# Optimization experiments

Hardware: AMD Instinct MI355X
Metric: run time of the kernel (lower is better)

The kernel has to match this reference:

```python
import jax, jax.numpy as jnp
import numpy as np

E = 768       # embed dim
NH = 12       # heads
HD = 64       # head dim
WIN = 14      # window size
DEPTH = 12
PATCH = 16
WINDOW_IDX = (0, 1, 3, 4, 6, 7, 9, 10)
EPS = 1e-6


def layer_norm(x, w, b):
    mu = jnp.mean(x, axis=-1, keepdims=True)
    var = jnp.mean(jnp.square(x - mu), axis=-1, keepdims=True)
    return (x - mu) * jax.lax.rsqrt(var + EPS) * w + b


def get_rel_pos(size, rel_pos):
    # q_size == k_size -> direct lookup, no interpolation
    coords = jnp.arange(size)
    rel = coords[:, None] - coords[None, :] + (size - 1)
    return rel_pos[rel]  # (size, size, HD)


def attention(x, qkv_w, qkv_b, proj_w, proj_b, rel_h, rel_w):
    B, H, W, _ = x.shape
    N = H * W
    qkv = (x.reshape(B, N, E) @ qkv_w + qkv_b).reshape(B, N, 3, NH, HD)
    q = qkv[:, :, 0].transpose(0, 2, 1, 3).reshape(B * NH, N, HD)
    k = qkv[:, :, 1].transpose(0, 2, 1, 3).reshape(B * NH, N, HD)
    v = qkv[:, :, 2].transpose(0, 2, 1, 3).reshape(B * NH, N, HD)
    attn = (q * (HD ** -0.5)) @ k.transpose(0, 2, 1)  # (B*NH, N, N)
    # decomposed relative position bias
    Rh = get_rel_pos(H, rel_h)  # (H, H, HD)
    Rw = get_rel_pos(W, rel_w)  # (W, W, HD)
    r_q = q.reshape(B * NH, H, W, HD)
    rh = jnp.einsum('bhwc,hkc->bhwk', r_q, Rh)
    rw = jnp.einsum('bhwc,wkc->bhwk', r_q, Rw)
    attn = attn.reshape(B * NH, H, W, H, W) + rh[:, :, :, :, None] + rw[:, :, :, None, :]
    attn = jax.nn.softmax(attn.reshape(B * NH, N, N), axis=-1)
    out = (attn @ v).reshape(B, NH, H, W, HD).transpose(0, 2, 3, 1, 4).reshape(B, H, W, E)
    return out @ proj_w + proj_b


def window_partition(x, ws):
    B, H, W, C = x.shape
    pad_h, pad_w = (-H) % ws, (-W) % ws
    x = jnp.pad(x, ((0, 0), (0, pad_h), (0, pad_w), (0, 0)))
    Hp, Wp = H + pad_h, W + pad_w
    x = x.reshape(B, Hp // ws, ws, Wp // ws, ws, C).transpose(0, 1, 3, 2, 4, 5)
    return x.reshape(-1, ws, ws, C), (Hp, Wp)


def window_unpartition(win, ws, pad_hw, hw):
    Hp, Wp = pad_hw
    H, W = hw
    B = win.shape[0] // ((Hp // ws) * (Wp // ws))
    x = win.reshape(B, Hp // ws, Wp // ws, ws, ws, -1).transpose(0, 1, 3, 2, 4, 5)
    return x.reshape(B, Hp, Wp, -1)[:, :H, :W]


def _forward(x, patch_w, patch_b, pos_embed,
             ln1_w, ln1_b, qkv_w, qkv_b, proj_w, proj_b,
             rel_h_win, rel_w_win, rel_h_glob, rel_w_glob,
             ln2_w, ln2_b, fc1_w, fc1_b, fc2_w, fc2_b, out_w, out_b):
    # patch embed: conv 16x16 stride 16
    x = jax.lax.conv_general_dilated(
        x, patch_w, (PATCH, PATCH), 'VALID',
        dimension_numbers=('NCHW', 'OIHW', 'NCHW'))
    x = x.transpose(0, 2, 3, 1) + patch_b  # (B, H, W, C)
    x = x + pos_embed
    win_i, glob_i = 0, 0
    for i in range(DEPTH):
        shortcut = x
        h = layer_norm(x, ln1_w[i], ln1_b[i])
        if i in WINDOW_IDX:
            hw = h.shape[1:3]
            h, pad_hw = window_partition(h, WIN)
            h = attention(h, qkv_w[i], qkv_b[i], proj_w[i], proj_b[i],
                          rel_h_win[win_i], rel_w_win[win_i])
            h = window_unpartition(h, WIN, pad_hw, hw)
            win_i += 1
        else:
            h = attention(h, qkv_w[i], qkv_b[i], proj_w[i], proj_b[i],
                          rel_h_glob[glob_i], rel_w_glob[glob_i])
            glob_i += 1
        x = shortcut + h
        h = layer_norm(x, ln2_w[i], ln2_b[i])
        h = jax.nn.gelu(h @ fc1_w[i] + fc1_b[i], approximate=False) @ fc2_w[i] + fc2_b[i]
        x = x + h
    feat = x.transpose(0, 3, 1, 2)  # (B, C, H, W) == 'last_feat'
    return jnp.einsum('bchw,oc->bohw', feat, out_w) + out_b[None, :, None, None]


def setup_inputs() -> dict:
    key = jax.random.key(0)
    ks = iter(jax.random.split(key, 64))
    def n(shape, s=0.02):
        return jax.random.normal(next(ks), shape, jnp.float32) * s
    B, IMG = 2, 512
    G = IMG // PATCH  # 32
    return {
        'x': jax.random.normal(next(ks), (B, 3, IMG, IMG), jnp.float32),
        'patch_w': n((E, 3, PATCH, PATCH)),
        'patch_b': jnp.zeros((E,), jnp.float32),
        'pos_embed': n((1, G, G, E)),
        'ln1_w': jnp.ones((DEPTH, E), jnp.float32),
        'ln1_b': jnp.zeros((DEPTH, E), jnp.float32),
        'qkv_w': n((DEPTH, E, 3 * E)),
        'qkv_b': jnp.zeros((DEPTH, 3 * E), jnp.float32),
        'proj_w': n((DEPTH, E, E)),
        'proj_b': jnp.zeros((DEPTH, E), jnp.float32),
        'rel_h_win': n((8, 2 * WIN - 1, HD)),
        'rel_w_win': n((8, 2 * WIN - 1, HD)),
        'rel_h_glob': n((4, 2 * G - 1, HD)),
        'rel_w_glob': n((4, 2 * G - 1, HD)),
        'ln2_w': jnp.ones((DEPTH, E), jnp.float32),
        'ln2_b': jnp.zeros((DEPTH, E), jnp.float32),
        'fc1_w': n((DEPTH, E, 4 * E)),
        'fc1_b': jnp.zeros((DEPTH, 4 * E), jnp.float32),
        'fc2_w': n((DEPTH, 4 * E, E)),
        'fc2_b': jnp.zeros((DEPTH, E), jnp.float32),
        'out_w': n((256, E)),
        'out_b': jnp.zeros((256,), jnp.float32),
    }


def reference(x, patch_w, patch_b, pos_embed,
              ln1_w, ln1_b, qkv_w, qkv_b, proj_w, proj_b,
              rel_h_win, rel_w_win, rel_h_glob, rel_w_glob,
              ln2_w, ln2_b, fc1_w, fc1_b, fc2_w, fc2_b, out_w, out_b):
    return _forward(x, patch_w, patch_b, pos_embed,
                    ln1_w, ln1_b, qkv_w, qkv_b, proj_w, proj_b,
                    rel_h_win, rel_w_win, rel_h_glob, rel_w_glob,
                    ln2_w, ln2_b, fc1_w, fc1_b, fc2_w, fc2_b, out_w, out_b)
```

## Files before the change

kernel.cpp:

```cpp
#include <hip/hip_runtime.h>
#include <hip/hip_bf16.h>
#include <math.h>

static constexpr int E   = 768;
static constexpr int NH  = 12;
static constexpr int HD  = 64;
static constexpr int Bsz = 2;
static constexpr int G   = 32;
static constexpr int NTOK = G * G;
static constexpr int ROWS = Bsz * NTOK;
static constexpr int WS  = 14;
static constexpr int NWIN_SIDE = 3;
static constexpr int NWIN = NWIN_SIDE * NWIN_SIDE;
static constexpr int BW  = Bsz * NWIN;
static constexpr int NW  = WS * WS;
static constexpr int WROWS = BW * NW;
static constexpr int WIN_MASK = 0x6DB;

typedef __attribute__((ext_vector_type(8))) short short8;
typedef __attribute__((ext_vector_type(4))) float f32x4;
typedef unsigned short ushort_t;

__device__ __forceinline__ unsigned short f2bf(float x) {
  union { float f; unsigned u; } v; v.f = x;
  unsigned r = v.u + 0x7fffu + ((v.u >> 16) & 1u);
  return (unsigned short)(r >> 16);
}
__device__ __forceinline__ float bf2f(unsigned short h) {
  union { unsigned u; float f; } v; v.u = ((unsigned)h) << 16;
  return v.f;
}

__device__ __forceinline__ void glds16(const void* g, void* l) {
  __builtin_amdgcn_global_load_lds(
      (const __attribute__((address_space(1))) unsigned*)g,
      (__attribute__((address_space(3))) unsigned*)l, 16, 0, 0);
}

__global__ __launch_bounds__(256) void ln_kernel(
    const float* __restrict__ in, const float* __restrict__ w,
    const float* __restrict__ b, ushort_t* __restrict__ out) {
  const int wave = threadIdx.x >> 6, lane = threadIdx.x & 63;
  const int row = blockIdx.x * 4 + wave;
  const float4* r4 = (const float4*)(in + (size_t)row * E);
  float4 v[3];
  v[0] = r4[lane]; v[1] = r4[lane + 64]; v[2] = r4[lane + 128];
  float s = 0.f, s2 = 0.f;
#pragma unroll
  for (int i = 0; i < 3; i++) {
    s += v[i].x + v[i].y + v[i].z + v[i].w;
    s2 += v[i].x * v[i].x + v[i].y * v[i].y + v[i].z * v[i].z + v[i].w * v[i].w;
  }
#pragma unroll
  for (int off = 1; off <= 32; off <<= 1) {
    s += __shfl_xor(s, off);
    s2 += __shfl_xor(s2, off);
  }
  const float mean = s * (1.f / E);
  const float var  = s2 * (1.f / E) - mean * mean;
  const float rs   = rsqrtf(var + 1e-6f);
  ushort_t* o = out + (size_t)row * E;
#pragma unroll
  for (int i = 0; i < 3; i++) {
    const int e0 = (lane + i * 64) * 4;
    ushort4 p;
    p.x = f2bf((v[i].x - mean) * rs * w[e0]     + b[e0]);
    p.y = f2bf((v[i].y - mean) * rs * w[e0 + 1] + b[e0 + 1]);
    p.z = f2bf((v[i].z - mean) * rs * w[e0 + 2] + b[e0 + 2]);
    p.w = f2bf((v[i].w - mean) * rs * w[e0 + 3] + b[e0 + 3]);
    *(ushort4*)&o[e0] = p;
  }
}

enum { OP_QKV = 0, OP_GELU = 1, OP_ADD = 2, OP_POS = 3, OP_HEAD = 4 };

template <int OP>
__global__ __launch_bounds__(256) void gemm_128(
    const ushort_t* __restrict__ A, const ushort_t* __restrict__ Bt,
    const float* __restrict__ bias, const float* __restrict__ res,
    const float* __restrict__ pos, void* __restrict__ Cp,
    int M, int N, int K, int ncol) {
  __shared__ ushort_t As[128 * 64];
  __shared__ ushort_t Bs[128 * 64];
  const int tid = threadIdx.x, wave = tid >> 6, lane = tid & 63;
  const int lx = lane & 15, ly = lane >> 4;

  const int nwg = gridDim.x;
  const int q = nwg >> 3, r = nwg & 7;
  const int xcd = blockIdx.x & 7, loc = blockIdx.x >> 3;
  const int wgid = ((xcd < r) ? xcd * (q + 1) : r * (q + 1) + (xcd - r) * q) + loc;
  const int brow = wgid / ncol, bcol = wgid - brow * ncol;
  const int row0 = brow * 128, col0 = bcol * 128;
  const int wm = (wave >> 1) * 64, wn = (wave & 1) * 64;
  const int rin = lane >> 3, pseg = lane & 7;
  const int lseg = pseg ^ rin;
  f32x4 acc[4][4] = {};

  const ushort_t* aptr[4];
  const ushort_t* bptr[4];
#pragma unroll
  for (int j = 0; j < 4; j++) {
    const int instr = wave * 4 + j;
    int ar = row0 + instr * 8 + rin;
    if (ar >= M) ar = M - 1;
    aptr[j] = &A[(size_t)ar * K + lseg * 8];
    const int br = col0 + instr * 8 + rin;
    bptr[j] = &Bt[(size_t)br * K + lseg * 8];
  }

  for (int k0 = 0; k0 < K; k0 += 64) {
    __syncthreads();
#pragma unroll
    for (int j = 0; j < 4; j++) {
      const int instr = wave * 4 + j;
      glds16(aptr[j] + k0, &As[instr * 512]);
      glds16(bptr[j] + k0, &Bs[instr * 512]);
    }
    __syncthreads();
#pragma unroll
    for (int kb = 0; kb < 2; kb++) {
      short8 af[4], bfm[4];
#pragma unroll
      for (int m = 0; m < 4; m++) {
        const int rr = wm + m * 16 + lx;
        af[m] = *(const short8*)&As[rr * 64 + (((kb * 4 + ly) ^ (rr & 7)) * 8)];
      }
#pragma unroll
      for (int n = 0; n < 4; n++) {
        const int rr = wn + n * 16 + lx;
        bfm[n] = *(const short8*)&Bs[rr * 64 + (((kb * 4 + ly) ^ (rr & 7)) * 8)];
      }
      __builtin_amdgcn_s_setprio(1);
#pragma unroll
      for (int m = 0; m < 4; m++)
#pragma unroll
        for (int n = 0; n < 4; n++)
          acc[m][n] = __builtin_amdgcn_mfma_f32_16x16x32_bf16(af[m], bfm[n], acc[m][n], 0, 0, 0);
      __builtin_amdgcn_s_setprio(0);
    }
  }

#pragma unroll
  for (int m = 0; m < 4; m++) {
#pragma unroll
    for (int r4 = 0; r4 < 4; r4++) {
      const int gr = row0 + wm + m * 16 + ly * 4 + r4;
      if (gr >= M) continue;
#pragma unroll
      for (int n = 0; n < 4; n++) {
        const int gc = col0 + wn + n * 16 + lx;
        float v = acc[m][n][r4] + bias[gc];
        if (OP == OP_GELU) v = 0.5f * v * (1.f + erff(v * 0.70710678118654752f));
        if (OP == OP_ADD)  v += res[(size_t)gr * N + gc];
        if (OP == OP_QKV || OP == OP_GELU)
          ((ushort_t*)Cp)[(size_t)gr * N + gc] = f2bf(v);
        else
          ((float*)Cp)[(size_t)gr * N + gc] = v;
      }
    }
  }
}

template <int OP, int MAP>
__global__ __launch_bounds__(256) void gemm_bt(
    const ushort_t* __restrict__ A, const ushort_t* __restrict__ Bt,
    const float* __restrict__ bias, const float* __restrict__ res,
    const float* __restrict__ pos, void* __restrict__ Cp,
    int M, int N, int K, int ncol) {
  __shared__ ushort_t As[2][64 * 64];
  __shared__ ushort_t Bs[2][64 * 64];
  const int tid = threadIdx.x, wave = tid >> 6, lane = tid & 63;
  const int lx = lane & 15, ly = lane >> 4;

  const int nwg = gridDim.x;
  const int q = nwg >> 3, r = nwg & 7;
  const int xcd = blockIdx.x & 7, loc = blockIdx.x >> 3;
  const int wgid = ((xcd < r) ? xcd * (q + 1) : r * (q + 1) + (xcd - r) * q) + loc;
  const int brow = wgid / ncol, bcol = wgid - brow * ncol;
  const int row0 = brow * 64, col0 = bcol * 64;
  const int wm = (wave >> 1) * 32, wn = (wave & 1) * 32;
  const int rin = lane >> 3, pseg = lane & 7;
  const int lseg = pseg ^ rin;
  f32x4 acc[2][2] = {};

  const ushort_t* aptr[2];
  const ushort_t* bptr[2];
#pragma unroll
  for (int j = 0; j < 2; j++) {
    const int slot = wave * 2 + j;
    int ar = row0 + slot * 8 + rin;
    if (ar >= M) ar = M - 1;
    if (MAP == 2) {
      const int bI = ar >> 10, t = ar & 1023, y = t >> 5, x = t & 31;
      const int by = y / WS, wy = y - by * WS;
      const int bx = x / WS, wx = x - bx * WS;
      const int win = bI * NWIN + by * NWIN_SIDE + bx;
      aptr[j] = &A[((size_t)win * NW + wy * WS + wx) * E + lseg * 8];
    } else {
      aptr[j] = &A[(size_t)ar * K + lseg * 8];
    }
    const int br = col0 + slot * 8 + rin;
    bptr[j] = &Bt[(size_t)br * K + lseg * 8];
  }

#pragma unroll
  for (int j = 0; j < 2; j++) {
    const int slot = wave * 2 + j;
    glds16(aptr[j], &As[0][slot * 512]);
    glds16(bptr[j], &Bs[0][slot * 512]);
  }

  const int nt = K >> 6;
  for (int t = 0; t < nt; t++) {
    const int cur = t & 1;
    if (t + 1 < nt) {
      const int k1 = (t + 1) << 6;
#pragma unroll
      for (int j = 0; j < 2; j++) {
        const int slot = wave * 2 + j;
        glds16(aptr[j] + k1, &As[cur ^ 1][slot * 512]);
        glds16(bptr[j] + k1, &Bs[cur ^ 1][slot * 512]);
      }
      asm volatile("s_waitcnt vmcnt(4)" ::: "memory");
    } else {
      asm volatile("s_waitcnt vmcnt(0)" ::: "memory");
    }
    __builtin_amdgcn_s_barrier();
    __builtin_amdgcn_sched_barrier(0);
#pragma unroll
    for (int kb = 0; kb < 2; kb++) {
      short8 af[2], bfm[2];
#pragma unroll
      for (int m = 0; m < 2; m++) {
        const int rr = wm + m * 16 + lx;
        af[m] = *(const short8*)&As[cur][rr * 64 + (((kb * 4 + ly) ^ (rr & 7)) * 8)];
      }
#pragma unroll
      for (int n = 0; n < 2; n++) {
        const int rr = wn + n * 16 + lx;
        bfm[n] = *(const short8*)&Bs[cur][rr * 64 + (((kb * 4 + ly) ^ (rr & 7)) * 8)];
      }
      __builtin_amdgcn_s_setprio(1);
#pragma unroll
      for (int m = 0; m < 2; m++)
#pragma unroll
        for (int n = 0; n < 2; n++)
          acc[m][n] = __builtin_amdgcn_mfma_f32_16x16x32_bf16(af[m], bfm[n], acc[m][n], 0, 0, 0);
      __builtin_amdgcn_s_setprio(0);
    }
    asm volatile("s_waitcnt lgkmcnt(0)" ::: "memory");
    __builtin_amdgcn_s_barrier();
    __builtin_amdgcn_sched_barrier(0);
  }

#pragma unroll
  for (int m = 0; m < 2; m++) {
#pragma unroll
    for (int r4 = 0; r4 < 4; r4++) {
      const int gr = row0 + wm + m * 16 + ly * 4 + r4;
      if (gr >= M) continue;
#pragma unroll
      for (int n = 0; n < 2; n++) {
        const int gc = col0 + wn + n * 16 + lx;
        float v = acc[m][n][r4] + bias[gc];
        if (OP == OP_GELU) v = 0.5f * v * (1.f + erff(v * 0.70710678118654752f));
        if (OP == OP_ADD)  v += res[(size_t)gr * N + gc];
        if (OP == OP_POS)  v += pos[(size_t)(gr & 1023) * N + gc];
        if (OP == OP_QKV || OP == OP_GELU)
          ((ushort_t*)Cp)[(size_t)gr * N + gc] = f2bf(v);
        else if (OP == OP_HEAD)
          ((float*)Cp)[(((size_t)(gr >> 10) * 256 + gc) << 10) | (gr & 1023)] = v;
        else
          ((float*)Cp)[(size_t)gr * N + gc] = v;
      }
    }
  }
}

__global__ __launch_bounds__(128) void attn_mfma(
    const ushort_t* __restrict__ qkv, ushort_t* __restrict__ out,
    const float* __restrict__ relh, const float* __restrict__ relw,
    int Hd, int Wd) {
  const int Ntok = Hd * Wd;
  __shared__ ushort_t smem[11392];
  ushort_t* Ks   = smem;
  ushort_t* Vst  = smem + 2048;
  ushort_t* Ps   = smem + 4608;
  ushort_t* Qs   = smem;
  ushort_t* RelS = smem + 2048;
  ushort_t* Th   = smem + 6144;
  ushort_t* Tw   = smem + 8256;
  ushort_t* khw  = smem + 10368;

  const int tid = threadIdx.x, wave = tid >> 6, lane = tid & 63;
  const int lx = lane & 15, ly = lane >> 4;
  const int bh = blockIdx.y, b = bh / NH, nh = bh % NH;
  const int q0 = blockIdx.x * 32;
  const size_t base = (size_t)b * Ntok * 2304 + nh * 64;

#pragma unroll
  for (int i = 0; i < 2; i++) {
    const int fv = i * 128 + tid;
    const int row = fv >> 3, dv8 = (fv & 7) * 8;
    const int qq = min(q0 + row, Ntok - 1);
    short8 v = *(const short8*)&qkv[base + (size_t)qq * 2304 + dv8];
    *(short8*)&Qs[(row * 64 + dv8) ^ ((row & 7) << 3)] = v;
  }
  for (int k = tid; k < 1024; k += 128) {
    const int kc = min(k, Ntok - 1);
    const int kh = kc / Wd;
    khw[k] = (ushort_t)((kh << 8) | (kc - kh * Wd));
  }
  __syncthreads();

  short8 qa[2];
  {
    const int row = wave * 16 + lx;
#pragma unroll
    for (int kb = 0; kb < 2; kb++)
      qa[kb] = *(const short8*)&Qs[(row * 64 + kb * 32 + ly * 8) ^ ((row & 7) << 3)];
  }
  int qh_r[4], qw_r[4];
#pragma unroll
  for (int r = 0; r < 4; r++) {
    const int qc = min(q0 + wave * 16 + ly * 4 + r, Ntok - 1);
    qh_r[r] = qc / Wd;
    qw_r[r] = qc - qh_r[r] * Wd;
  }

  for (int t = 0; t < 2; t++) {
    const float* rel = t ? relw : relh;
    const int TR = t ? (2 * Wd - 1) : (2 * Hd - 1);
    __syncthreads();
#pragma unroll
    for (int i = 0; i < 4; i++) {
      const int fv = i * 128 + tid;
      const int row = fv >> 3, c8 = (fv & 7) * 8;
      short8 v = {};
      if (row < TR) {
        const float* rp = &rel[(size_t)row * 64 + c8];
        const float4 a = *(const float4*)rp;
        const float4 bq = *(const float4*)(rp + 4);
        v[0] = (short)f2bf(a.x);  v[1] = (short)f2bf(a.y);
        v[2] = (short)f2bf(a.z);  v[3] = (short)f2bf(a.w);
        v[4] = (short)f2bf(bq.x); v[5] = (short)f2bf(bq.y);
        v[6] = (short)f2bf(bq.z); v[7] = (short)f2bf(bq.w);
      }
      *(short8*)&RelS[(row * 64 + c8) ^ ((row & 7) << 3)] = v;
    }
    __syncthreads();
    const int NT = (TR + 15) >> 4;
    ushort_t* T = t ? Tw : Th;
    for (int nt = 0; nt < NT; nt++) {
      f32x4 a = {};
      __builtin_amdgcn_s_setprio(1);
#pragma unroll
      for (int kb = 0; kb < 2; kb++) {
        const int rrow = nt * 16 + lx;
        short8 bfv = *(const short8*)&RelS[(rrow * 64 + kb * 32 + ly * 8) ^ ((rrow & 7) << 3)];
        a = __builtin_amdgcn_mfma_f32_16x16x32_bf16(qa[kb], bfv, a, 0, 0, 0);
      }
      __builtin_amdgcn_s_setprio(0);
#pragma unroll
      for (int reg = 0; reg < 4; reg++)
        T[(wave * 16 + ly * 4 + reg) * 66 + nt * 16 + lx] = f2bf(a[reg]);
    }
  }

  f32x4 o[4] = {};
  float m_[4], l_[4];
#pragma unroll
  for (int r = 0; r < 4; r++) { m_[r] = -3e38f; l_[r] = 0.f; }

  const int nkt = (Ntok + 31) >> 5;
  const int srow = tid >> 3, c7 = tid & 7, dv8s = c7 * 8;
  const int vswz = (c7 & 3) << 3;

  short8 kpre[2], vpre[2];
#pragma unroll
  for (int i = 0; i < 2; i++) {
    const int gk = srow + i * 16;
    short8 kv = {}, vv = {};
    if (gk < Ntok) {
      kv = *(const short8*)&qkv[base + 768 + (size_t)gk * 2304 + dv8s];
      vv = *(const short8*)&qkv[base + 1536 + (size_t)gk * 2304 + dv8s];
    }
    kpre[i] = kv; vpre[i] = vv;
  }

  for (int kt = 0; kt < nkt; kt++) {
    __syncthreads();
#pragma unroll
    for (int i = 0; i < 2; i++) {
      const int row = srow + i * 16;
      *(short8*)&Ks[(row * 64 + dv8s) ^ ((row & 7) << 3)] = kpre[i];
      const int kcol = row ^ vswz;
#pragma unroll
      for (int j = 0; j < 8; j++)
        Vst[(dv8s + j) * 40 + kcol] = (ushort_t)vpre[i][j];
    }
    if (kt + 1 < nkt) {
#pragma unroll
      for (int i = 0; i < 2; i++) {
        const int gk = (kt + 1) * 32 + srow + i * 16;
        short8 kv = {}, vv = {};
        if (gk < Ntok) {
          kv = *(const short8*)&qkv[base + 768 + (size_t)gk * 2304 + dv8s];
          vv = *(const short8*)&qkv[base + 1536 + (size_t)gk * 2304 + dv8s];
        }
        kpre[i] = kv; vpre[i] = vv;
      }
    }
    __syncthreads();

    f32x4 c[2] = {};
    __builtin_amdgcn_s_setprio(1);
#pragma unroll
    for (int kb = 0; kb < 2; kb++)
#pragma unroll
      for (int ct = 0; ct < 2; ct++) {
        const int krow = ct * 16 + lx;
        short8 kf = *(const short8*)&Ks[(krow * 64 + kb * 32 + ly * 8) ^ ((krow & 7) << 3)];
        c[ct] = __builtin_amdgcn_mfma_f32_16x16x32_bf16(qa[kb], kf, c[ct], 0, 0, 0);
      }
    __builtin_amdgcn_s_setprio(0);

    const int k0a = kt * 32 + lx, k1a = k0a + 16;
    const int tv0 = khw[k0a], tv1 = khw[k1a];
    const int kh0 = tv0 >> 8, kw0 = tv0 & 255;
    const int kh1 = tv1 >> 8, kw1 = tv1 & 255;
    float pv0[4], pv1[4], mt[4];
#pragma unroll
    for (int r = 0; r < 4; r++) {
      const int trow = (wave * 16 + ly * 4 + r) * 66;
      float s0 = c[0][r] * 0.125f + bf2f(Th[trow + qh_r[r] - kh0 + Hd - 1])
               + bf2f(Tw[trow + qw_r[r] - kw0 + Wd - 1]);
      float s1 = c[1][r] * 0.125f + bf2f(Th[trow + qh_r[r] - kh1 + Hd - 1])
               + bf2f(Tw[trow + qw_r[r] - kw1 + Wd - 1]);
      if (k0a >= Ntok) s0 = -1e30f;
      if (k1a >= Ntok) s1 = -1e30f;
      pv0[r] = s0; pv1[r] = s1;
      mt[r] = fmaxf(s0, s1);
    }
    const float dmax = fmaxf(fmaxf(mt[0] - m_[0], mt[1] - m_[1]),
                             fmaxf(mt[2] - m_[2], mt[3] - m_[3]));
    if (!__all(dmax <= 8.f)) {
#pragma unroll
      for (int r = 0; r < 4; r++) {
        float mr = mt[r];
#pragma unroll
        for (int off = 1; off <= 8; off <<= 1) mr = fmaxf(mr, __shfl_xor(mr, off));
        const float mn = fmaxf(m_[r], mr);
        const float sc = __expf(m_[r] - mn);
        m_[r] = mn; l_[r] *= sc;
#pragma unroll
        for (int dt = 0; dt < 4; dt++) o[dt][r] *= sc;
      }
    }
#pragma unroll
    for (int r = 0; r < 4; r++) {
      const float p0 = __expf(pv0[r] - m_[r]);
      const float p1 = __expf(pv1[r] - m_[r]);
      l_[r] += p0 + p1;
      const int pb = wave * 640 + (ly * 4 + r) * 40;
      Ps[pb + lx]      = f2bf(p0);
      Ps[pb + 16 + lx] = f2bf(p1);
    }
    short8 pf = *(const short8*)&Ps[wave * 640 + lx * 40 + ly * 8];
    __builtin_amdgcn_s_setprio(1);
#pragma unroll
    for (int dt = 0; dt < 4; dt++) {
      const int drow = dt * 16 + lx;
      short8 vf = *(const short8*)&Vst[drow * 40 + ((ly * 8) ^ (((drow >> 3) & 3) << 3))];
      o[dt] = __builtin_amdgcn_mfma_f32_16x16x32_bf16(pf, vf, o[dt], 0, 0, 0);
    }
    __builtin_amdgcn_s_setprio(0);
  }

#pragma unroll
  for (int r = 0; r < 4; r++) {
#pragma unroll
    for (int off = 1; off <= 8; off <<= 1) l_[r] += __shfl_xor(l_[r], off);
    const int qq = q0 + wave * 16 + ly * 4 + r;
    if (qq >= Ntok) continue;
    const float inv = 1.f / l_[r];
#pragma unroll
    for (int dt = 0; dt < 4; dt++)
      out[((size_t)b * Ntok + qq) * E + nh * 64 + dt * 16 + lx] = f2bf(o[dt][r] * inv);
  }
}

__global__ __launch_bounds__(128) void qkv_winpart(
    const ushort_t* __restrict__ qi, const float* __restrict__ qkvb,
    ushort_t* __restrict__ qw) {
  const int row = blockIdx.x;
  const int win = row / NW, t = row - win * NW;
  const int wy = t / WS, wx = t - wy * WS;
  const int b = win / NWIN, wr = win - b * NWIN;
  const int by = wr / NWIN_SIDE, bx = wr - by * NWIN_SIDE;
  const int y = by * WS + wy, x = bx * WS + wx;
  short8* dst = (short8*)(qw + (size_t)row * 2304);
  if (y < G && x < G) {
    const short8* src = (const short8*)(qi + (((size_t)b * G + y) * G + x) * 2304);
    for (int e = threadIdx.x; e < 288; e += 128) dst[e] = src[e];
  } else {
    for (int e = threadIdx.x; e < 288; e += 128) {
      short8 v;
#pragma unroll
      for (int j = 0; j < 8; j++) v[j] = (short)f2bf(qkvb[e * 8 + j]);
      dst[e] = v;
    }
  }
}

__global__ __launch_bounds__(256) void im2col(const float* __restrict__ x,
                                              ushort_t* __restrict__ out) {
  const int blk = blockIdx.x;
  const int b = blk >> 10, t = blk & 1023, gy = t >> 5, gx = t & 31;
  for (int k = threadIdx.x; k < 768; k += 256) {
    const int ci = k >> 8, rem = k & 255, py = rem >> 4, px = rem & 15;
    out[(size_t)blk * 768 + k] =
        f2bf(x[(((size_t)b * 3 + ci) * 512 + gy * 16 + py) * 512 + gx * 16 + px]);
  }
}

__global__ __launch_bounds__(256) void prep_wt64(
    const float* __restrict__ qkvw, const float* __restrict__ projw,
    const float* __restrict__ fc1w, const float* __restrict__ fc2w,
    ushort_t* __restrict__ wq, ushort_t* __restrict__ wp,
    ushort_t* __restrict__ w1, ushort_t* __restrict__ w2) {
  __shared__ float tile[64][65];
  const int blk = blockIdx.x;
  const float* W; ushort_t* Wt; int Kd, Nd, tn, tk;
  if (blk < 432)       { W = qkvw;  Wt = wq; Kd = 768;  Nd = 2304; tn = blk % 36;          tk = blk / 36; }
  else if (blk < 576)  { W = projw; Wt = wp; Kd = 768;  Nd = 768;  tn = (blk - 432) % 12;  tk = (blk - 432) / 12; }
  else if (blk < 1152) { W = fc1w;  Wt = w1; Kd = 768;  Nd = 3072; tn = (blk - 576) % 48;  tk = (blk - 576) / 48; }
  else                 { W = fc2w;  Wt = w2; Kd = 3072; Nd = 768;  tn = (blk - 1152) % 12; tk = (blk - 1152) / 12; }
  const int k0 = tk * 64, n0 = tn * 64;
  const int kr = threadIdx.x >> 2, cg = (threadIdx.x & 3) * 16;
  const float* src = &W[(size_t)(k0 + kr) * Nd + n0 + cg];
#pragma unroll
  for (int j = 0; j < 4; j++) {
    const float4 v = *(const float4*)&src[j * 4];
    tile[kr][cg + j * 4 + 0] = v.x;
    tile[kr][cg + j * 4 + 1] = v.y;
    tile[kr][cg + j * 4 + 2] = v.z;
    tile[kr][cg + j * 4 + 3] = v.w;
  }
  __syncthreads();
  const int nr = kr;
  short8 o0, o1;
#pragma unroll
  for (int j = 0; j < 8; j++) o0[j] = (short)f2bf(tile[cg + j][nr]);
#pragma unroll
  for (int j = 0; j < 8; j++) o1[j] = (short)f2bf(tile[cg + 8 + j][nr]);
  ushort_t* dst = &Wt[(size_t)(n0 + nr) * Kd + k0 + cg];
  *(short8*)&dst[0] = o0;
  *(short8*)&dst[8] = o1;
}

__global__ __launch_bounds__(256) void cast_bf16(const float* __restrict__ in,
                                                 ushort_t* __restrict__ out, int n) {
  const int idx = (blockIdx.x * 256 + threadIdx.x) * 4;
  if (idx + 3 < n) {
    const float4 v = *(const float4*)&in[idx];
    ushort4 p;
    p.x = f2bf(v.x); p.y = f2bf(v.y); p.z = f2bf(v.z); p.w = f2bf(v.w);
    *(ushort4*)&out[idx] = p;
  }
}

extern "C" void kernel_launch(void* const* d_in, const int* in_sizes, int n_in,
                              void* d_out, int out_size, void* d_ws, size_t ws_size,
                              hipStream_t stream) {
  const float* x_in     = (const float*)d_in[0];
  const float* patch_w  = (const float*)d_in[1];
  const float* patch_b  = (const float*)d_in[2];
  const float* pos_emb  = (const float*)d_in[3];
  const float* ln1_w    = (const float*)d_in[4];
  const float* ln1_b    = (const float*)d_in[5];
  const float* qkv_w    = (const float*)d_in[6];
  const float* qkv_b    = (const float*)d_in[7];
  const float* proj_w   = (const float*)d_in[8];
  const float* proj_b   = (const float*)d_in[9];
  const float* rel_h_w  = (const float*)d_in[10];
  const float* rel_w_w  = (const float*)d_in[11];
  const float* rel_h_g  = (const float*)d_in[12];
  const float* rel_w_g  = (const float*)d_in[13];
  const float* ln2_w    = (const float*)d_in[14];
  const float* ln2_b    = (const float*)d_in[15];
  const float* fc1_w    = (const float*)d_in[16];
  const float* fc1_b    = (const float*)d_in[17];
  const float* fc2_w    = (const float*)d_in[18];
  const float* fc2_b    = (const float*)d_in[19];
  const float* out_w    = (const float*)d_in[20];
  const float* out_b    = (const float*)d_in[21];
  float* outp = (float*)d_out;

  float* xbuf = (float*)d_ws;
  ushort_t* hb16    = (ushort_t*)(xbuf + (size_t)ROWS * E);
  ushort_t* qkvimg  = hb16 + (size_t)ROWS * E;
  ushort_t* qkvwin  = qkvimg + (size_t)ROWS * 3 * E;
  ushort_t* attnw16 = qkvwin + (size_t)WROWS * 3 * E;
  ushort_t* h1b16   = attnw16 + (size_t)WROWS * E;
  ushort_t* wq      = h1b16 + (size_t)ROWS * 4 * E;
  ushort_t* wp      = wq + (size_t)2304 * 768;
  ushort_t* w1      = wp + (size_t)768 * 768;
  ushort_t* w2      = w1 + (size_t)3072 * 768;
  ushort_t* pwT16   = w2 + (size_t)768 * 3072;
  ushort_t* headW16 = pwT16 + (size_t)768 * 768;
  ushort_t* imb16 = hb16;

  cast_bf16<<<576, 256, 0, stream>>>(patch_w, pwT16, 768 * 768);
  cast_bf16<<<192, 256, 0, stream>>>(out_w, headW16, 256 * 768);

  im2col<<<ROWS, 256, 0, stream>>>(x_in, imb16);
  gemm_bt<OP_POS, 0><<<12 * 32, 256, 0, stream>>>(
      imb16, pwT16, patch_b, nullptr, pos_emb, xbuf, ROWS, E, E, 12);

  int win_i = 0, glob_i = 0;
  for (int i = 0; i < 12; i++) {
    const bool is_win = (WIN_MASK >> i) & 1;

    prep_wt64<<<1728, 256, 0, stream>>>(
        qkv_w + (size_t)i * E * 3 * E, proj_w + (size_t)i * E * E,
        fc1_w + (size_t)i * E * 4 * E, fc2_w + (size_t)i * 4 * E * E,
        wq, wp, w1, w2);

    ln_kernel<<<ROWS / 4, 256, 0, stream>>>(xbuf, ln1_w + i * E, ln1_b + i * E, hb16);

    gemm_128<OP_QKV><<<288, 256, 0, stream>>>(
        hb16, wq, qkv_b + i * 3 * E, nullptr, nullptr, qkvimg, ROWS, 3 * E, E, 18);

    if (is_win) {
      qkv_winpart<<<WROWS, 128, 0, stream>>>(qkvimg, qkv_b + i * 3 * E, qkvwin);
      attn_mfma<<<dim3(7, BW * NH), 128, 0, stream>>>(
          qkvwin, attnw16, rel_h_w + (size_t)win_i * (2 * WS - 1) * HD,
          rel_w_w + (size_t)win_i * (2 * WS - 1) * HD, WS, WS);
      win_i++;
      gemm_bt<OP_ADD, 2><<<12 * 32, 256, 0, stream>>>(
          attnw16, wp, proj_b + i * E, xbuf, nullptr, xbuf, ROWS, E, E, 12);
    } else {
      attn_mfma<<<dim3(32, Bsz * NH), 128, 0, stream>>>(
          qkvimg, attnw16, rel_h_g + (size_t)glob_i * (2 * G - 1) * HD,
          rel_w_g + (size_t)glob_i * (2 * G - 1) * HD, G, G);
      glob_i++;
      gemm_bt<OP_ADD, 0><<<12 * 32, 256, 0, stream>>>(
          attnw16, wp, proj_b + i * E, xbuf, nullptr, xbuf, ROWS, E, E, 12);
    }

    ln_kernel<<<ROWS / 4, 256, 0, stream>>>(xbuf, ln2_w + i * E, ln2_b + i * E, hb16);
    gemm_128<OP_GELU><<<384, 256, 0, stream>>>(
        hb16, w1, fc1_b + i * 4 * E, nullptr, nullptr, h1b16, ROWS, 4 * E, E, 24);
    gemm_bt<OP_ADD, 0><<<12 * 32, 256, 0, stream>>>(
        h1b16, w2, fc2_b + i * E, xbuf, nullptr, xbuf, ROWS, E, 4 * E, 12);
  }

  cast_bf16<<<1536, 256, 0, stream>>>(xbuf, hb16, ROWS * E);
  gemm_bt<OP_HEAD, 0><<<4 * 32, 256, 0, stream>>>(
      hb16, headW16, out_b, nullptr, nullptr, outp, ROWS, 256, E, 4);
}
```

Baseline: 1.842 ms.

## Use smaller GEMM tiles for more workgroups on narrow GEMMs

Drops the 128x128 single-buffered GEMM and runs QKV and FC1 on the double-buffered 64x64 kernel instead. Adds a 32x64-tile, 2-wave, double-buffered GEMM for the N=768 and N=256 GEMMs (patch embed, proj, fc2, head), doubling their workgroup count. The aim is to fill all CUs and overlap loads with MFMA on GEMMs that previously launched too few workgroups. In exchange each tile reuses operands less and makes more global and LDS traffic.

```diff
diff --git a/kernel.cpp b/kernel.cpp
--- a/kernel.cpp
+++ b/kernel.cpp
@@ -74,93 +74,6 @@
 
 enum { OP_QKV = 0, OP_GELU = 1, OP_ADD = 2, OP_POS = 3, OP_HEAD = 4 };
 
-template <int OP>
-__global__ __launch_bounds__(256) void gemm_128(
-    const ushort_t* __restrict__ A, const ushort_t* __restrict__ Bt,
-    const float* __restrict__ bias, const float* __restrict__ res,
-    const float* __restrict__ pos, void* __restrict__ Cp,
-    int M, int N, int K, int ncol) {
-  __shared__ ushort_t As[128 * 64];
-  __shared__ ushort_t Bs[128 * 64];
-  const int tid = threadIdx.x, wave = tid >> 6, lane = tid & 63;
-  const int lx = lane & 15, ly = lane >> 4;
-
-  const int nwg = gridDim.x;
-  const int q = nwg >> 3, r = nwg & 7;
-  const int xcd = blockIdx.x & 7, loc = blockIdx.x >> 3;
-  const int wgid = ((xcd < r) ? xcd * (q + 1) : r * (q + 1) + (xcd - r) * q) + loc;
-  const int brow = wgid / ncol, bcol = wgid - brow * ncol;
-  const int row0 = brow * 128, col0 = bcol * 128;
-  const int wm = (wave >> 1) * 64, wn = (wave & 1) * 64;
-  const int rin = lane >> 3, pseg = lane & 7;
-  const int lseg = pseg ^ rin;
-  f32x4 acc[4][4] = {};
-
-  const ushort_t* aptr[4];
-  const ushort_t* bptr[4];
-#pragma unroll
-  for (int j = 0; j < 4; j++) {
-    const int instr = wave * 4 + j;
-    int ar = row0 + instr * 8 + rin;
-    if (ar >= M) ar = M - 1;
-    aptr[j] = &A[(size_t)ar * K + lseg * 8];
-    const int br = col0 + instr * 8 + rin;
-    bptr[j] = &Bt[(size_t)br * K + lseg * 8];
-  }
-
-  for (int k0 = 0; k0 < K; k0 += 64) {
-    __syncthreads();
-#pragma unroll
-    for (int j = 0; j < 4; j++) {
-      const int instr = wave * 4 + j;
-      glds16(aptr[j] + k0, &As[instr * 512]);
-      glds16(bptr[j] + k0, &Bs[instr * 512]);
-    }
-    __syncthreads();
-#pragma unroll
-    for (int kb = 0; kb < 2; kb++) {
-      short8 af[4], bfm[4];
-#pragma unroll
-      for (int m = 0; m < 4; m++) {
-        const int rr = wm + m * 16 + lx;
-        af[m] = *(const short8*)&As[rr * 64 + (((kb * 4 + ly) ^ (rr & 7)) * 8)];
-      }
-#pragma unroll
-      for (int n = 0; n < 4; n++) {
-        const int rr = wn + n * 16 + lx;
-        bfm[n] = *(const short8*)&Bs[rr * 64 + (((kb * 4 + ly) ^ (rr & 7)) * 8)];
-      }
-      __builtin_amdgcn_s_setprio(1);
-#pragma unroll
-      for (int m = 0; m < 4; m++)
-#pragma unroll
-        for (int n = 0; n < 4; n++)
-          acc[m][n] = __builtin_amdgcn_mfma_f32_16x16x32_bf16(af[m], bfm[n], acc[m][n], 0, 0, 0);
-      __builtin_amdgcn_s_setprio(0);
-    }
-  }
-
-#pragma unroll
-  for (int m = 0; m < 4; m++) {
-#pragma unroll
-    for (int r4 = 0; r4 < 4; r4++) {
-      const int gr = row0 + wm + m * 16 + ly * 4 + r4;
-      if (gr >= M) continue;
-#pragma unroll
-      for (int n = 0; n < 4; n++) {
-        const int gc = col0 + wn + n * 16 + lx;
-        float v = acc[m][n][r4] + bias[gc];
-        if (OP == OP_GELU) v = 0.5f * v * (1.f + erff(v * 0.70710678118654752f));
-        if (OP == OP_ADD)  v += res[(size_t)gr * N + gc];
-        if (OP == OP_QKV || OP == OP_GELU)
-          ((ushort_t*)Cp)[(size_t)gr * N + gc] = f2bf(v);
-        else
-          ((float*)Cp)[(size_t)gr * N + gc] = v;
-      }
-    }
-  }
-}
-
 template <int OP, int MAP>
 __global__ __launch_bounds__(256) void gemm_bt(
     const ushort_t* __restrict__ A, const ushort_t* __restrict__ Bt,
@@ -258,6 +171,122 @@
 #pragma unroll
     for (int r4 = 0; r4 < 4; r4++) {
       const int gr = row0 + wm + m * 16 + ly * 4 + r4;
+      if (gr >= M) continue;
+#pragma unroll
+      for (int n = 0; n < 2; n++) {
+        const int gc = col0 + wn + n * 16 + lx;
+        float v = acc[m][n][r4] + bias[gc];
+        if (OP == OP_GELU) v = 0.5f * v * (1.f + erff(v * 0.70710678118654752f));
+        if (OP == OP_ADD)  v += res[(size_t)gr * N + gc];
+        if (OP == OP_POS)  v += pos[(size_t)(gr & 1023) * N + gc];
+        if (OP == OP_QKV || OP == OP_GELU)
+          ((ushort_t*)Cp)[(size_t)gr * N + gc] = f2bf(v);
+        else if (OP == OP_HEAD)
+          ((float*)Cp)[(((size_t)(gr >> 10) * 256 + gc) << 10) | (gr & 1023)] = v;
+        else
+          ((float*)Cp)[(size_t)gr * N + gc] = v;
+      }
+    }
+  }
+}
+
+template <int OP, int MAP>
+__global__ __launch_bounds__(128) void gemm_32(
+    const ushort_t* __restrict__ A, const ushort_t* __restrict__ Bt,
+    const float* __restrict__ bias, const float* __restrict__ res,
+    const float* __restrict__ pos, void* __restrict__ Cp,
+    int M, int N, int K, int ncol) {
+  __shared__ ushort_t As[2][32 * 64];
+  __shared__ ushort_t Bs[2][64 * 64];
+  const int tid = threadIdx.x, wave = tid >> 6, lane = tid & 63;
+  const int lx = lane & 15, ly = lane >> 4;
+
+  const int nwg = gridDim.x;
+  const int q = nwg >> 3, r = nwg & 7;
+  const int xcd = blockIdx.x & 7, loc = blockIdx.x >> 3;
+  const int wgid = ((xcd < r) ? xcd * (q + 1) : r * (q + 1) + (xcd - r) * q) + loc;
+  const int brow = wgid / ncol, bcol = wgid - brow * ncol;
+  const int row0 = brow * 32, col0 = bcol * 64;
+  const int wn = wave * 32;
+  const int rin = lane >> 3, pseg = lane & 7;
+  const int lseg = pseg ^ rin;
+  f32x4 acc[2][2] = {};
+
+  const ushort_t* aptr[2];
+  const ushort_t* bptr[4];
+#pragma unroll
+  for (int j = 0; j < 2; j++) {
+    const int slot = wave * 2 + j;
+    int ar = row0 + slot * 8 + rin;
+    if (ar >= M) ar = M - 1;
+    if (MAP == 2) {
+      const int bI = ar >> 10, t = ar & 1023, y = t >> 5, x = t & 31;
+      const int by = y / WS, wy = y - by * WS;
+      const int bx = x / WS, wx = x - bx * WS;
+      const int win = bI * NWIN + by * NWIN_SIDE + bx;
+      aptr[j] = &A[((size_t)win * NW + wy * WS + wx) * E + lseg * 8];
+    } else {
+      aptr[j] = &A[(size_t)ar * K + lseg * 8];
+    }
+  }
+#pragma unroll
+  for (int j = 0; j < 4; j++) {
+    const int slot = wave * 4 + j;
+    const int br = col0 + slot * 8 + rin;
+    bptr[j] = &Bt[(size_t)br * K + lseg * 8];
+  }
+
+#pragma unroll
+  for (int j = 0; j < 2; j++) glds16(aptr[j], &As[0][(wave * 2 + j) * 512]);
+#pragma unroll
+  for (int j = 0; j < 4; j++) glds16(bptr[j], &Bs[0][(wave * 4 + j) * 512]);
+
+  const int nt = K >> 6;
+  for (int t = 0; t < nt; t++) {
+    const int cur = t & 1;
+    if (t + 1 < nt) {
+      const int k1 = (t + 1) << 6;
+#pragma unroll
+      for (int j = 0; j < 2; j++) glds16(aptr[j] + k1, &As[cur ^ 1][(wave * 2 + j) * 512]);
+#pragma unroll
+      for (int j = 0; j < 4; j++) glds16(bptr[j] + k1, &Bs[cur ^ 1][(wave * 4 + j) * 512]);
+      asm volatile("s_waitcnt vmcnt(6)" ::: "memory");
+    } else {
+      asm volatile("s_waitcnt vmcnt(0)" ::: "memory");
+    }
+    __builtin_amdgcn_s_barrier();
+    __builtin_amdgcn_sched_barrier(0);
+#pragma unroll
+    for (int kb = 0; kb < 2; kb++) {
+      short8 af[2], bfm[2];
+#pragma unroll
+      for (int m = 0; m < 2; m++) {
+        const int rr = m * 16 + lx;
+        af[m] = *(const short8*)&As[cur][rr * 64 + (((kb * 4 + ly) ^ (rr & 7)) * 8)];
+      }
+#pragma unroll
+      for (int n = 0; n < 2; n++) {
+        const int rr = wn + n * 16 + lx;
+        bfm[n] = *(const short8*)&Bs[cur][rr * 64 + (((kb * 4 + ly) ^ (rr & 7)) * 8)];
+      }
+      __builtin_amdgcn_s_setprio(1);
+#pragma unroll
+      for (int m = 0; m < 2; m++)
+#pragma unroll
+        for (int n = 0; n < 2; n++)
+          acc[m][n] = __builtin_amdgcn_mfma_f32_16x16x32_bf16(af[m], bfm[n], acc[m][n], 0, 0, 0);
+      __builtin_amdgcn_s_setprio(0);
+    }
+    asm volatile("s_waitcnt lgkmcnt(0)" ::: "memory");
+    __builtin_amdgcn_s_barrier();
+    __builtin_amdgcn_sched_barrier(0);
+  }
+
+#pragma unroll
+  for (int m = 0; m < 2; m++) {
+#pragma unroll
+    for (int r4 = 0; r4 < 4; r4++) {
+      const int gr = row0 + m * 16 + ly * 4 + r4;
       if (gr >= M) continue;
 #pragma unroll
       for (int n = 0; n < 2; n++) {
@@ -615,7 +644,7 @@
   cast_bf16<<<192, 256, 0, stream>>>(out_w, headW16, 256 * 768);
 
   im2col<<<ROWS, 256, 0, stream>>>(x_in, imb16);
-  gemm_bt<OP_POS, 0><<<12 * 32, 256, 0, stream>>>(
+  gemm_32<OP_POS, 0><<<768, 128, 0, stream>>>(
       imb16, pwT16, patch_b, nullptr, pos_emb, xbuf, ROWS, E, E, 12);
 
   int win_i = 0, glob_i = 0;
@@ -629,8 +658,8 @@
 
     ln_kernel<<<ROWS / 4, 256, 0, stream>>>(xbuf, ln1_w + i * E, ln1_b + i * E, hb16);
 
-    gemm_128<OP_QKV><<<288, 256, 0, stream>>>(
-        hb16, wq, qkv_b + i * 3 * E, nullptr, nullptr, qkvimg, ROWS, 3 * E, E, 18);
+    gemm_bt<OP_QKV, 0><<<36 * 32, 256, 0, stream>>>(
+        hb16, wq, qkv_b + i * 3 * E, nullptr, nullptr, qkvimg, ROWS, 3 * E, E, 36);
 
     if (is_win) {
       qkv_winpart<<<WROWS, 128, 0, stream>>>(qkvimg, qkv_b + i * 3 * E, qkvwin);
@@ -638,25 +667,25 @@
           qkvwin, attnw16, rel_h_w + (size_t)win_i * (2 * WS - 1) * HD,
           rel_w_w + (size_t)win_i * (2 * WS - 1) * HD, WS, WS);
       win_i++;
-      gemm_bt<OP_ADD, 2><<<12 * 32, 256, 0, stream>>>(
+      gemm_32<OP_ADD, 2><<<768, 128, 0, stream>>>(
           attnw16, wp, proj_b + i * E, xbuf, nullptr, xbuf, ROWS, E, E, 12);
     } else {
       attn_mfma<<<dim3(32, Bsz * NH), 128, 0, stream>>>(
           qkvimg, attnw16, rel_h_g + (size_t)glob_i * (2 * G - 1) * HD,
           rel_w_g + (size_t)glob_i * (2 * G - 1) * HD, G, G);
       glob_i++;
-      gemm_bt<OP_ADD, 0><<<12 * 32, 256, 0, stream>>>(
+      gemm_32<OP_ADD, 0><<<768, 128, 0, stream>>>(
           attnw16, wp, proj_b + i * E, xbuf, nullptr, xbuf, ROWS, E, E, 12);
     }
 
     ln_kernel<<<ROWS / 4, 256, 0, stream>>>(xbuf, ln2_w + i * E, ln2_b + i * E, hb16);
-    gemm_128<OP_GELU><<<384, 256, 0, stream>>>(
-        hb16, w1, fc1_b + i * 4 * E, nullptr, nullptr, h1b16, ROWS, 4 * E, E, 24);
-    gemm_bt<OP_ADD, 0><<<12 * 32, 256, 0, stream>>>(
+    gemm_bt<OP_GELU, 0><<<48 * 32, 256, 0, stream>>>(
+        hb16, w1, fc1_b + i * 4 * E, nullptr, nullptr, h1b16, ROWS, 4 * E, E, 48);
+    gemm_32<OP_ADD, 0><<<768, 128, 0, stream>>>(
         h1b16, w2, fc2_b + i * E, xbuf, nullptr, xbuf, ROWS, E, 4 * E, 12);
   }
 
   cast_bf16<<<1536, 256, 0, stream>>>(xbuf, hb16, ROWS * E);
-  gemm_bt<OP_HEAD, 0><<<4 * 32, 256, 0, stream>>>(
+  gemm_32<OP_HEAD, 0><<<256, 128, 0, stream>>>(
       hb16, headW16, out_b, nullptr, nullptr, outp, ROWS, 256, E, 4);
 }
```

After: 1.807 ms. No clear change (-1.9%).
